# Kernel optimization log

Measured on AMD Instinct MI355X. Metric: run time of the kernel, lower is better.

Reference implementation:

```python
import jax, jax.numpy as jnp
import numpy as np

N_DATASETS = 2
DATASET_CATS = (1536, 1536)
TOTAL_CATS = 3072
MAX_UNIFY = 1536
N_NODES = TOTAL_CATS + MAX_UNIFY  # 4608
LRELU_ALPHA = 0.2
BI_TEMP = 0.05
NEG_INF = -9e15


def setup_inputs() -> dict:
    key = jax.random.key(0)
    ks = jax.random.split(key, 12)
    nfeat, nfeat_out, nfeat_adj, nhid, nheads = 512, 256, 64, 64, 4
    att_out, mlp = 256, 512
    s = lambda k, sh: (jax.random.normal(k, sh, jnp.float32) * 0.05)
    return {
        'x': jax.random.normal(ks[0], (N_NODES, nfeat), jnp.float32),
        'W_before': s(ks[1], (nfeat, nfeat_out)),
        'b_before': jnp.zeros((nfeat_out,), jnp.float32),
        'W_adj': s(ks[2], (nfeat_out, nfeat_adj)),
        'b_adj': jnp.zeros((nfeat_adj,), jnp.float32),
        'W_heads': s(ks[3], (nheads, nfeat_out, nhid)),
        'a_heads': s(ks[4], (nheads, 2 * nhid)),
        'W_out': s(ks[5], (nheads * nhid, att_out)),
        'a_out': s(ks[6], (2 * att_out,)),
        'W_lin1': s(ks[7], (att_out, mlp)),
        'b_lin1': jnp.zeros((mlp,), jnp.float32),
    }


def _calc_adjacency(x_out, W_adj, b_adj):
    # linear_adj + L2 normalize + cosine similarity + row normalization via diag(1/rowsum)
    af = x_out @ W_adj + b_adj                              # [N, nfeat_adj]
    nrm = jnp.sqrt(jnp.sum(af * af, axis=1, keepdims=True))
    naf = af / jnp.maximum(nrm, 1e-12)
    sim = naf @ naf.T                                       # [N, N]
    rowsum = jnp.sum(sim, axis=1)
    r_inv = 1.0 / rowsum
    r_inv = jnp.where(jnp.isinf(r_inv), 0.0, r_inv)
    return r_inv[:, None] * sim                             # diag(1/rowsum) @ sim


def _gat_multihead(x, adj, W, a):
    # W: [H, F, d], a: [H, 2d]. Standard pyGAT dense attention, vectorized over heads.
    d = W.shape[-1]
    Wh = jnp.einsum('nf,hfd->hnd', x, W)                    # [H, N, d]
    f1 = jnp.einsum('hnd,hd->hn', Wh, a[:, :d])             # [H, N]
    f2 = jnp.einsum('hnd,hd->hn', Wh, a[:, d:])             # [H, N]
    e = jax.nn.leaky_relu(f1[:, :, None] + f2[:, None, :], LRELU_ALPHA)  # [H, N, N]
    att = jnp.where(adj[None] > 0, e, NEG_INF)
    att = jax.nn.softmax(att, axis=-1)
    return jnp.einsum('hnm,hmd->hnd', att, Wh)              # [H, N, d]


def _gat_single(x, adj, W, a):
    d = W.shape[-1]
    Wh = x @ W                                              # [N, d]
    f1 = Wh @ a[:d]
    f2 = Wh @ a[d:]
    e = jax.nn.leaky_relu(f1[:, None] + f2[None, :], LRELU_ALPHA)
    att = jnp.where(adj > 0, e, NEG_INF)
    att = jax.nn.softmax(att, axis=-1)
    return att @ Wh


def reference(x, W_before, b_before, W_adj, b_adj, W_heads, a_heads, W_out, a_out, W_lin1, b_lin1):
    x1 = x @ W_before + b_before                            # linear_before
    adj = _calc_adjacency(x1, W_adj, b_adj)                 # before relu, as in source
    x1 = jax.nn.relu(x1)
    # multi-head GAT layer 1 (concat=True -> elu per head, concat along feature dim)
    h = jax.nn.elu(_gat_multihead(x1, adj, W_heads, a_heads))   # [H, N, d]
    H, N, d = h.shape
    feat = jnp.transpose(h, (1, 0, 2)).reshape(N, H * d)
    x2 = feat + x1                                          # residual; dropout is eval no-op
    # output attention head (concat=False -> no elu inside)
    x3 = jax.nn.elu(_gat_single(x2, adj, W_out, a_out) + x2)
    feat_mlp = x3 @ W_lin1 + b_lin1                          # linear1
    # sep_bipartite_graphs: per-dataset column-softmax over unify columns
    bgs = []
    cur = 0
    for nc in DATASET_CATS:
        blk = adj[cur:cur + nc, TOTAL_CATS:]                 # [nc, MAX_UNIFY]
        bgs.append(jax.nn.softmax(blk / BI_TEMP, axis=0))
        cur += nc
    return (feat_mlp[TOTAL_CATS:],) + tuple(bgs)


if __name__ == '__main__':
    out = reference(**setup_inputs())
    for o in out:
        print(o.shape, o.dtype)
```

## Files before the change

### kernel.cpp

```cpp
#include <hip/hip_runtime.h>
#include <hip/hip_bf16.h>
#include <math.h>

constexpr int NTOT = 4608;
constexpr int TC   = 3072;
constexpr int MU   = 1536;
constexpr int NH   = 4;

constexpr long OFF_ADJ  = 0;
constexpr long OFF_X1   = OFF_ADJ  + (long)NTOT*NTOT;
constexpr long OFF_NAF  = OFF_X1   + (long)NTOT*256;
constexpr long OFF_PART = OFF_NAF  + (long)NTOT*64;
constexpr long OFF_RINV = OFF_PART + 72*64;
constexpr long OFF_WH   = OFF_RINV + NTOT;
constexpr long OFF_F1H  = OFF_WH   + (long)4*NTOT*64;
constexpr long OFF_F2H  = OFF_F1H  + (long)4*NTOT;
constexpr long OFF_MXH  = OFF_F2H  + (long)4*NTOT;
constexpr long OFF_CIH  = OFF_MXH  + (long)4*NTOT;
constexpr long OFF_X2   = OFF_CIH  + (long)4*NTOT;
constexpr long OFF_WH2  = OFF_X2   + (long)NTOT*256;
constexpr long OFF_F1S  = OFF_WH2  + (long)NTOT*256;
constexpr long OFF_F2S  = OFF_F1S  + NTOT;
constexpr long OFF_MXS  = OFF_F2S  + NTOT;
constexpr long OFF_CIS  = OFF_MXS  + NTOT;
constexpr long OFF_X3   = OFF_CIS  + NTOT;
constexpr long OFF_PMAX = OFF_X3   + (long)MU*256;
constexpr long OFF_PSUM = OFF_PMAX + (long)2*12*MU;
constexpr long OFF_FMAX = OFF_PSUM + (long)2*12*MU;
constexpr long OFF_FIS  = OFF_FMAX + (long)2*MU;
constexpr long OFF_L1   = OFF_FIS  + (long)2*MU;
constexpr long OFF_L2   = OFF_L1   + (long)4*NTOT;
constexpr long OFF_PARTS = OFF_ADJ + (long)TC*NTOT;
constexpr long OFF_POSB  = OFF_PARTS + 2L*NTOT*36;
constexpr long OFF_MASKB = OFF_POSB  + 2L*NTOT*72;

typedef __attribute__((ext_vector_type(8))) short bf16x8;
typedef __attribute__((ext_vector_type(8))) unsigned short ushort8;
typedef __attribute__((ext_vector_type(4))) float floatx4;

__device__ __forceinline__ float elu(float x)   { return (x > 0.f) ? x : expm1f(x); }
__device__ __forceinline__ unsigned short f2bf(float f) {
    unsigned u = __float_as_uint(f);
    u += 0x7FFFu + ((u >> 16) & 1u);
    return (unsigned short)(u >> 16);
}

__global__ __launch_bounds__(256) void zero2_k(
    float* __restrict__ a, long na4, float* __restrict__ b, long nb4)
{
    long i = (long)blockIdx.x * 256 + threadIdx.x;
    float4 z = make_float4(0.f, 0.f, 0.f, 0.f);
    if (i < na4) *(float4*)(a + i * 4) = z;
    else {
        long j = i - na4;
        if (j < nb4) *(float4*)(b + j * 4) = z;
    }
}

template<bool RELU_A, bool BIAS>
__global__ __launch_bounds__(256) void gemm_rm(
    const float* __restrict__ A, const float* __restrict__ B,
    const float* __restrict__ bias, float* __restrict__ C,
    int K, int M, long strideBz, long strideCz)
{
    __shared__ float As[16][68];
    __shared__ float Bs[16][68];
    const float* Bz = B + (long)blockIdx.z * strideBz;
    float* Cz = C + (long)blockIdx.z * strideCz;
    int tid = threadIdx.x;
    int r0 = blockIdx.x * 64;
    int c0 = blockIdx.y * 64;
    int ty = tid >> 4, tx = tid & 15;
    int srow = tid >> 2, skg = tid & 3;
    int bkk = tid >> 4, bc4 = (tid & 15) * 4;
    const float* Arow = A + (long)(r0 + srow) * K + skg * 4;
    float4 aReg = *(const float4*)(Arow);
    float4 bReg = *(const float4*)&Bz[(long)bkk * M + c0 + bc4];
    float acc[4][4] = {};
    for (int k0 = 0; k0 < K; k0 += 16) {
        {
            float4 v = aReg;
            if (RELU_A) {
                v.x = fmaxf(v.x, 0.f); v.y = fmaxf(v.y, 0.f);
                v.z = fmaxf(v.z, 0.f); v.w = fmaxf(v.w, 0.f);
            }
            As[skg * 4 + 0][srow] = v.x;
            As[skg * 4 + 1][srow] = v.y;
            As[skg * 4 + 2][srow] = v.z;
            As[skg * 4 + 3][srow] = v.w;
            *(float4*)&Bs[bkk][bc4] = bReg;
        }
        __syncthreads();
        if (k0 + 16 < K) {
            aReg = *(const float4*)(Arow + k0 + 16);
            bReg = *(const float4*)&Bz[(long)(k0 + 16 + bkk) * M + c0 + bc4];
        }
        #pragma unroll
        for (int kk = 0; kk < 16; ++kk) {
            float4 av = *(const float4*)&As[kk][ty * 4];
            float4 bv = *(const float4*)&Bs[kk][tx * 4];
            float a[4] = { av.x, av.y, av.z, av.w };
            float b[4] = { bv.x, bv.y, bv.z, bv.w };
            #pragma unroll
            for (int i = 0; i < 4; ++i)
                #pragma unroll
                for (int j = 0; j < 4; ++j) acc[i][j] += a[i] * b[j];
        }
        __syncthreads();
    }
    #pragma unroll
    for (int i = 0; i < 4; ++i) {
        int r = r0 + ty * 4 + i;
        #pragma unroll
        for (int j = 0; j < 4; ++j) {
            int c = c0 + tx * 4 + j;
            float v = acc[i][j];
            if (BIAS) v += bias[c];
            Cz[(long)r * M + c] = v;
        }
    }
}

__global__ __launch_bounds__(256) void af_naf(
    const float* __restrict__ x1, const float* __restrict__ W_adj,
    const float* __restrict__ b_adj, float* __restrict__ nafT)
{
    __shared__ float rowbuf[4][256];
    int tid = threadIdx.x, w = tid >> 6, lane = tid & 63;
    int n = blockIdx.x * 4 + w;
    #pragma unroll
    for (int l = 0; l < 4; ++l) rowbuf[w][l * 64 + lane] = x1[(long)n * 256 + l * 64 + lane];
    __syncthreads();
    float acc = b_adj[lane];
    for (int k = 0; k < 256; ++k) acc += rowbuf[w][k] * W_adj[k * 64 + lane];
    float sq = acc * acc;
    #pragma unroll
    for (int off = 32; off >= 1; off >>= 1) sq += __shfl_xor(sq, off);
    float nrm = fmaxf(sqrtf(sq), 1e-12f);
    nafT[(long)lane * NTOT + n] = acc / nrm;
}

__global__ __launch_bounds__(256) void sim_k8(
    const float* __restrict__ nafT, float* __restrict__ sim,
    double* __restrict__ parts, unsigned long long* __restrict__ posb)
{
    __shared__ float As[32][128];
    __shared__ float Bs[32][128];
    __shared__ unsigned char sgn[128][2][16];
    int tid = threadIdx.x;
    int n0 = blockIdx.x * 128, m0 = blockIdx.y * 128;
    int ty = tid >> 4, tx = tid & 15;
    float acc[2][2][4][4] = {};
    for (int ks = 0; ks < 2; ++ks) {
        if (ks) __syncthreads();
        int k0 = ks * 32;
        #pragma unroll
        for (int l = 0; l < 4; ++l) {
            int idx = l * 256 + tid;
            int kk = idx >> 5, f4 = idx & 31;
            *(float4*)&As[kk][f4 * 4] = *(const float4*)&nafT[(long)(k0 + kk) * NTOT + n0 + f4 * 4];
            *(float4*)&Bs[kk][f4 * 4] = *(const float4*)&nafT[(long)(k0 + kk) * NTOT + m0 + f4 * 4];
        }
        __syncthreads();
        for (int kk = 0; kk < 32; ++kk) {
            float4 av0 = *(const float4*)&As[kk][ty * 4];
            float4 av1 = *(const float4*)&As[kk][64 + ty * 4];
            float4 bv0 = *(const float4*)&Bs[kk][tx * 4];
            float4 bv1 = *(const float4*)&Bs[kk][64 + tx * 4];
            float a[2][4] = { { av0.x, av0.y, av0.z, av0.w }, { av1.x, av1.y, av1.z, av1.w } };
            float b[2][4] = { { bv0.x, bv0.y, bv0.z, bv0.w }, { bv1.x, bv1.y, bv1.z, bv1.w } };
            #pragma unroll
            for (int rh = 0; rh < 2; ++rh)
                #pragma unroll
                for (int ch = 0; ch < 2; ++ch)
                    #pragma unroll
                    for (int i = 0; i < 4; ++i)
                        #pragma unroll
                        for (int j = 0; j < 4; ++j)
                            acc[rh][ch][i][j] += a[rh][i] * b[ch][j];
        }
    }
    if (m0 >= TC && n0 < TC) {
        #pragma unroll
        for (int rh = 0; rh < 2; ++rh)
            #pragma unroll
            for (int i = 0; i < 4; ++i) {
                long r = n0 + rh * 64 + ty * 4 + i;
                #pragma unroll
                for (int ch = 0; ch < 2; ++ch) {
                    float4 o = make_float4(acc[rh][ch][i][0], acc[rh][ch][i][1],
                                           acc[rh][ch][i][2], acc[rh][ch][i][3]);
                    *(float4*)(sim + r * NTOT + m0 + ch * 64 + tx * 4) = o;
                }
            }
    }
    int mt36 = m0 >> 7;
    #pragma unroll
    for (int rh = 0; rh < 2; ++rh)
        #pragma unroll
        for (int i = 0; i < 4; ++i) {
            double t = 0.0;
            #pragma unroll
            for (int ch = 0; ch < 2; ++ch)
                t += ((double)acc[rh][ch][i][0] + (double)acc[rh][ch][i][1])
                   + ((double)acc[rh][ch][i][2] + (double)acc[rh][ch][i][3]);
            #pragma unroll
            for (int off = 1; off < 16; off <<= 1) t += __shfl_xor(t, off);
            if (tx == 0)
                parts[(long)(n0 + rh * 64 + ty * 4 + i) * 36 + mt36] = t;
        }
    int mt = m0 >> 6;
    #pragma unroll
    for (int rh = 0; rh < 2; ++rh)
        #pragma unroll
        for (int i = 0; i < 4; ++i)
            #pragma unroll
            for (int ch = 0; ch < 2; ++ch) {
                unsigned nib = (unsigned)(acc[rh][ch][i][0] > 0.f)
                             | ((unsigned)(acc[rh][ch][i][1] > 0.f) << 1)
                             | ((unsigned)(acc[rh][ch][i][2] > 0.f) << 2)
                             | ((unsigned)(acc[rh][ch][i][3] > 0.f) << 3);
                sgn[rh * 64 + ty * 4 + i][ch][tx] = (unsigned char)nib;
            }
    __syncthreads();
    {
        int rl = tid >> 1, gh = tid & 1;
        unsigned long long w = 0;
        #pragma unroll
        for (int t = 0; t < 16; ++t)
            w |= (unsigned long long)sgn[rl][gh][t] << (4 * t);
        posb[(long)(n0 + rl) * 72 + mt + gh] = w;
    }
}

__global__ __launch_bounds__(256) void fused1(
    const float* __restrict__ Wh, unsigned short* __restrict__ Wf1,
    const float* __restrict__ a_heads,
    float* __restrict__ f1, float* __restrict__ f2,
    float* __restrict__ e2p, float* __restrict__ e2n,
    const double* __restrict__ parts, const unsigned long long* __restrict__ posb,
    float* __restrict__ rinv, unsigned long long* __restrict__ maskb)
{
    __shared__ float t[64][65];
    int b = blockIdx.x;
    int tid = threadIdx.x;
    if (b < 288) {
        int mt = b % 72, h = b / 72;
        int n0 = mt * 64;
        const float* inz = Wh + (long)h * NTOT * 64;
        int r4 = tid >> 6, k = tid & 63;
        #pragma unroll
        for (int l = 0; l < 16; ++l) {
            int row = l * 4 + r4;
            t[row][k] = inz[(long)(n0 + row) * 64 + k];
        }
        __syncthreads();
        #pragma unroll
        for (int q = 0; q < 2; ++q) {
            int fid = q * 256 + tid;
            int dt = fid >> 7, ks = (fid >> 6) & 1, lane = fid & 63;
            int mb = ks * 32 + (lane >> 4) * 8;
            int d  = dt * 16 + (lane & 15);
            ushort8 w;
            #pragma unroll
            for (int j = 0; j < 8; ++j) w[j] = f2bf(t[mb + j][d]);
            long idx = ((((long)(h * 72 + mt) * 4 + dt) * 2 + ks) * 64 + lane) * 8;
            *(ushort8*)&Wf1[idx] = w;
        }
    } else if (b < 288 + 4608) {
        int tb = b - 288;
        int xb = tb % 1152, h = tb / 1152;
        int w = tid >> 6, lane = tid & 63;
        int n = xb * 4 + w;
        const float* row = Wh + ((long)h * NTOT + n) * 64;
        const float* a1 = a_heads + (long)h * 128;
        const float* a2 = a1 + 64;
        float v = row[lane];
        float p1 = v * a1[lane];
        float p2 = v * a2[lane];
        #pragma unroll
        for (int off = 32; off >= 1; off >>= 1) { p1 += __shfl_xor(p1, off); p2 += __shfl_xor(p2, off); }
        if (lane == 0) {
            f1[(long)h * NTOT + n] = p1;
            f2[(long)h * NTOT + n] = p2;
            e2p[(long)h * NTOT + n] = __expf(p2);
            e2n[(long)h * NTOT + n] = __expf(0.2f * p2);
        }
    } else {
        int xb = b - (288 + 4608);
        int w = tid >> 6, lane = tid & 63;
        int n = xb * 4 + w;
        double s = (lane < 36) ? parts[(long)n * 36 + lane] : 0.0;
        #pragma unroll
        for (int off = 32; off >= 1; off >>= 1) s += __shfl_xor(s, off);
        float rs = (float)s;
        float r = 1.0f / rs;
        if (isinf(r)) r = 0.f;
        if (lane == 0) rinv[n] = r;
        unsigned long long pw = posb[(long)n * 72 + lane];
        unsigned long long mw = (r < 0.f) ? ~pw : pw;
        if (r == 0.f) mw = 0ull;
        maskb[(long)n * 72 + lane] = mw;
        if (lane < 8) {
            pw = posb[(long)n * 72 + 64 + lane];
            mw = (r < 0.f) ? ~pw : pw;
            if (r == 0.f) mw = 0ull;
            maskb[(long)n * 72 + 64 + lane] = mw;
        }
    }
}

__global__ __launch_bounds__(256) void fused2(
    const float* __restrict__ Wh2, unsigned short* __restrict__ Wf2,
    const float* __restrict__ a_out,
    float* __restrict__ f1, float* __restrict__ f2,
    float* __restrict__ e2p, float* __restrict__ e2n)
{
    __shared__ float t[64][65];
    int b = blockIdx.x;
    int tid = threadIdx.x;
    if (b < 288) {
        int mt = b % 72, by = b / 72;
        int n0 = mt * 64, d0 = by * 64;
        int r4 = tid >> 6, k = tid & 63;
        #pragma unroll
        for (int l = 0; l < 16; ++l) {
            int row = l * 4 + r4;
            t[row][k] = Wh2[(long)(n0 + row) * 256 + d0 + k];
        }
        __syncthreads();
        #pragma unroll
        for (int q = 0; q < 2; ++q) {
            int fid = q * 256 + tid;
            int ctl = fid >> 7, ks = (fid >> 6) & 1, lane = fid & 63;
            int mb = ks * 32 + (lane >> 4) * 8;
            int dl = ctl * 16 + (lane & 15);
            ushort8 w;
            #pragma unroll
            for (int j = 0; j < 8; ++j) w[j] = f2bf(t[mb + j][dl]);
            long idx = (((long)(mt * 16 + by * 4 + ctl) * 2 + ks) * 64 + lane) * 8;
            *(ushort8*)&Wf2[idx] = w;
        }
    } else {
        int xb = b - 288;
        int w = tid >> 6, lane = tid & 63;
        int n = xb * 4 + w;
        const float* row = Wh2 + (long)n * 256;
        const float* a1 = a_out;
        const float* a2 = a_out + 256;
        float p1 = 0.f, p2 = 0.f;
        #pragma unroll
        for (int l = 0; l < 4; ++l) {
            float v = row[l * 64 + lane];
            p1 += v * a1[l * 64 + lane];
            p2 += v * a2[l * 64 + lane];
        }
        #pragma unroll
        for (int off = 32; off >= 1; off >>= 1) { p1 += __shfl_xor(p1, off); p2 += __shfl_xor(p2, off); }
        if (lane == 0) {
            f1[n] = p1;
            f2[n] = p2;
            e2p[n] = __expf(p2);
            e2n[n] = __expf(0.2f * p2);
        }
    }
}

__global__ __launch_bounds__(256) void mh_attn(
    const unsigned long long* __restrict__ maskb,
    const float* __restrict__ f1,
    const float* __restrict__ e2p, const float* __restrict__ e2n,
    const unsigned short* __restrict__ Wf1, float* __restrict__ accb,
    float* __restrict__ lbuf)
{
    int tid = threadIdx.x;
    int wave = tid >> 6, lane = tid & 63;
    int n0 = blockIdx.x * 64;
    int h = blockIdx.y, ch = blockIdx.z;
    const float* Ep = e2p + (long)h * NTOT;
    const float* En = e2n + (long)h * NTOT;
    int arow = lane & 15, acol8 = (lane >> 4) * 8;
    int n = n0 + 16 * wave + arow;
    float r1 = f1[(long)h * NTOT + n];
    float e1p = __expf(r1), e1n = __expf(0.2f * r1);
    float lsum = 0.f;
    floatx4 acc[4] = {};
    for (int mt = ch * 12; mt < ch * 12 + 12; ++mt) {
        int m0 = mt * 64;
        bf16x8 bfr[2][4];
        #pragma unroll
        for (int ks = 0; ks < 2; ++ks)
            #pragma unroll
            for (int dt = 0; dt < 4; ++dt) {
                long idx = ((((long)(h * 72 + mt) * 4 + dt) * 2 + ks) * 64 + lane) * 8;
                bfr[ks][dt] = *(const bf16x8*)&Wf1[idx];
            }
        unsigned long long mw = maskb[(long)n * 72 + mt];
        bf16x8 afr[2];
        #pragma unroll
        for (int ks = 0; ks < 2; ++ks) {
            int mc = m0 + ks * 32 + acol8;
            float4 pv0 = *(const float4*)(Ep + mc);
            float4 pv1 = *(const float4*)(Ep + mc + 4);
            float4 nv0 = *(const float4*)(En + mc);
            float4 nv1 = *(const float4*)(En + mc + 4);
            unsigned bits = (unsigned)(mw >> (ks * 32 + acol8)) & 0xFFu;
            float fp[8] = { pv0.x, pv0.y, pv0.z, pv0.w, pv1.x, pv1.y, pv1.z, pv1.w };
            float fn[8] = { nv0.x, nv0.y, nv0.z, nv0.w, nv1.x, nv1.y, nv1.z, nv1.w };
            #pragma unroll
            for (int j = 0; j < 8; ++j) {
                float tp = e1p * fp[j];
                float tn = e1n * fn[j];
                float p = (tp >= 1.0f) ? tp : tn;
                p = ((bits >> j) & 1u) ? p : 0.f;
                lsum += p;
                afr[ks][j] = (short)f2bf(p);
            }
        }
        #pragma unroll
        for (int ks = 0; ks < 2; ++ks)
            #pragma unroll
            for (int dt = 0; dt < 4; ++dt)
                acc[dt] = __builtin_amdgcn_mfma_f32_16x16x32_bf16(afr[ks], bfr[ks][dt], acc[dt], 0, 0, 0);
    }
    lsum += __shfl_xor(lsum, 16);
    lsum += __shfl_xor(lsum, 32);
    if (lane < 16) atomicAdd(lbuf + (long)h * NTOT + n0 + 16 * wave + lane, lsum);
    int crow = n0 + 16 * wave + (lane >> 4) * 4;
    int ccol = h * 64 + (lane & 15);
    #pragma unroll
    for (int dt = 0; dt < 4; ++dt)
        #pragma unroll
        for (int r = 0; r < 4; ++r)
            atomicAdd(accb + (long)(crow + r) * 256 + ccol + dt * 16, acc[dt][r]);
}

__global__ __launch_bounds__(256) void mh_fin(
    const float* __restrict__ accb, const float* __restrict__ lbuf,
    float* __restrict__ x1, float* __restrict__ x2)
{
    long idx = ((long)blockIdx.x * 256 + threadIdx.x) * 4;
    long r = idx >> 8;
    int h = (int)((idx & 255) >> 6);
    float l = lbuf[(long)h * NTOT + r];
    float inv = (l > 0.f) ? 1.0f / l : 0.f;
    float4 a = *(const float4*)(accb + idx);
    float4 xv = *(const float4*)(x1 + idx);
    float4 o;
    o.x = elu(a.x * inv) + fmaxf(xv.x, 0.f);
    o.y = elu(a.y * inv) + fmaxf(xv.y, 0.f);
    o.z = elu(a.z * inv) + fmaxf(xv.z, 0.f);
    o.w = elu(a.w * inv) + fmaxf(xv.w, 0.f);
    *(float4*)(x2 + idx) = o;
    if (idx < (long)MU * 256)
        *(float4*)(x1 + idx) = make_float4(0.f, 0.f, 0.f, 0.f);
}

__global__ __launch_bounds__(256) void s_attn(
    const unsigned long long* __restrict__ maskb,
    const float* __restrict__ f1,
    const float* __restrict__ e2p, const float* __restrict__ e2n,
    const unsigned short* __restrict__ Wf2, float* __restrict__ accb,
    float* __restrict__ lbuf)
{
    int tid = threadIdx.x;
    int wave = tid >> 6, lane = tid & 63;
    int lr0 = blockIdx.x * 32;
    int by = blockIdx.y;
    int ch = blockIdx.z;
    int arow = lane & 15, acol8 = (lane >> 4) * 8;
    int rt = wave & 1;
    int dt0 = (wave >> 1) * 4;
    int n = TC + lr0 + 16 * rt + arow;
    float r1 = f1[n];
    float e1p = __expf(r1), e1n = __expf(0.2f * r1);
    float lsum = 0.f;
    floatx4 acc[4] = {};
    for (int mt = ch * 6; mt < ch * 6 + 6; ++mt) {
        int m0 = mt * 64;
        bf16x8 bfr[2][4];
        #pragma unroll
        for (int ks = 0; ks < 2; ++ks)
            #pragma unroll
            for (int t = 0; t < 4; ++t) {
                long idx = (((long)(mt * 16 + by * 8 + dt0 + t) * 2 + ks) * 64 + lane) * 8;
                bfr[ks][t] = *(const bf16x8*)&Wf2[idx];
            }
        unsigned long long mw = maskb[(long)n * 72 + mt];
        bf16x8 afr[2];
        #pragma unroll
        for (int ks = 0; ks < 2; ++ks) {
            int mc = m0 + ks * 32 + acol8;
            float4 pv0 = *(const float4*)(e2p + mc);
            float4 pv1 = *(const float4*)(e2p + mc + 4);
            float4 nv0 = *(const float4*)(e2n + mc);
            float4 nv1 = *(const float4*)(e2n + mc + 4);
            unsigned bits = (unsigned)(mw >> (ks * 32 + acol8)) & 0xFFu;
            float fp[8] = { pv0.x, pv0.y, pv0.z, pv0.w, pv1.x, pv1.y, pv1.z, pv1.w };
            float fn[8] = { nv0.x, nv0.y, nv0.z, nv0.w, nv1.x, nv1.y, nv1.z, nv1.w };
            #pragma unroll
            for (int j = 0; j < 8; ++j) {
                float tp = e1p * fp[j];
                float tn = e1n * fn[j];
                float p = (tp >= 1.0f) ? tp : tn;
                p = ((bits >> j) & 1u) ? p : 0.f;
                lsum += p;
                afr[ks][j] = (short)f2bf(p);
            }
        }
        #pragma unroll
        for (int ks = 0; ks < 2; ++ks)
            #pragma unroll
            for (int t = 0; t < 4; ++t)
                acc[t] = __builtin_amdgcn_mfma_f32_16x16x32_bf16(afr[ks], bfr[ks][t], acc[t], 0, 0, 0);
    }
    lsum += __shfl_xor(lsum, 16);
    lsum += __shfl_xor(lsum, 32);
    if (by == 0 && wave < 2 && lane < 16)
        atomicAdd(lbuf + lr0 + 16 * wave + lane, lsum);
    int crow = lr0 + 16 * rt + (lane >> 4) * 4;
    #pragma unroll
    for (int t = 0; t < 4; ++t) {
        int ccol = by * 128 + (dt0 + t) * 16 + (lane & 15);
        #pragma unroll
        for (int r = 0; r < 4; ++r)
            atomicAdd(accb + (long)(crow + r) * 256 + ccol, acc[t][r]);
    }
}

__global__ __launch_bounds__(256) void s_fin(
    const float* __restrict__ accb, const float* __restrict__ lbuf,
    const float* __restrict__ x2, float* __restrict__ x3)
{
    long idx = ((long)blockIdx.x * 256 + threadIdx.x) * 4;
    long r = idx >> 8;
    float l = lbuf[r];
    float inv = (l > 0.f) ? 1.0f / l : 0.f;
    float4 a = *(const float4*)(accb + idx);
    float4 xv = *(const float4*)(x2 + (long)TC * 256 + idx);
    float4 o;
    o.x = elu(a.x * inv + xv.x);
    o.y = elu(a.y * inv + xv.y);
    o.z = elu(a.z * inv + xv.z);
    o.w = elu(a.w * inv + xv.w);
    *(float4*)(x3 + idx) = o;
}

__global__ __launch_bounds__(256) void bi_partial(
    const float* __restrict__ sim, const float* __restrict__ rinv,
    float* __restrict__ pmax, float* __restrict__ psum)
{
    int c = blockIdx.x * 256 + threadIdx.x;
    int ch = blockIdx.y;
    int ds = blockIdx.z;
    float m = -3.0e38f, s = 0.f;
    int rbase = ds * MU + ch * 128;
    for (int r = 0; r < 128; ++r) {
        float a = sim[(long)(rbase + r) * NTOT + TC + c] * rinv[rbase + r];
        float v = a * 20.0f;
        if (v <= m) s += expf(v - m);
        else { s = s * expf(m - v) + 1.f; m = v; }
    }
    pmax[((long)ds * 12 + ch) * MU + c] = m;
    psum[((long)ds * 12 + ch) * MU + c] = s;
}

__global__ __launch_bounds__(256) void bi_combine(
    const float* __restrict__ pmax, const float* __restrict__ psum,
    float* __restrict__ fmax, float* __restrict__ fis)
{
    int b = blockIdx.x;
    int ds = b / 6, ct = b % 6;
    int c = ct * 256 + threadIdx.x;
    float m = -3.0e38f;
    for (int ch = 0; ch < 12; ++ch) m = fmaxf(m, pmax[((long)ds * 12 + ch) * MU + c]);
    float s = 0.f;
    for (int ch = 0; ch < 12; ++ch)
        s += psum[((long)ds * 12 + ch) * MU + c] * expf(pmax[((long)ds * 12 + ch) * MU + c] - m);
    fmax[ds * MU + c] = m;
    fis[ds * MU + c] = 1.0f / s;
}

__global__ __launch_bounds__(256) void bi_norm(
    const float* __restrict__ sim, const float* __restrict__ rinv,
    const float* __restrict__ fmax, const float* __restrict__ fis,
    float* __restrict__ outbg)
{
    int c = blockIdx.x * 256 + threadIdx.x;
    int ch = blockIdx.y;
    int ds = blockIdx.z;
    float m = fmax[ds * MU + c], inv = fis[ds * MU + c];
    long obase = (long)ds * MU * MU;
    int rbase = ch * 128;
    for (int r = 0; r < 128; ++r) {
        int row = ds * MU + rbase + r;
        float a = sim[(long)row * NTOT + TC + c] * rinv[row];
        float v = a * 20.0f;
        outbg[obase + (long)(rbase + r) * MU + c] = expf(v - m) * inv;
    }
}

extern "C" void kernel_launch(void* const* d_in, const int* in_sizes, int n_in,
                              void* d_out, int out_size, void* d_ws, size_t ws_size,
                              hipStream_t stream)
{
    const float* x        = (const float*)d_in[0];
    const float* W_before = (const float*)d_in[1];
    const float* b_before = (const float*)d_in[2];
    const float* W_adj    = (const float*)d_in[3];
    const float* b_adj    = (const float*)d_in[4];
    const float* W_heads  = (const float*)d_in[5];
    const float* a_heads  = (const float*)d_in[6];
    const float* W_out    = (const float*)d_in[7];
    const float* a_out    = (const float*)d_in[8];
    const float* W_lin1   = (const float*)d_in[9];
    const float* b_lin1   = (const float*)d_in[10];
    float* out = (float*)d_out;
    float* ws  = (float*)d_ws;

    float* sim  = ws + OFF_ADJ;
    float* x1p  = ws + OFF_X1;
    float* nafT = ws + OFF_NAF;
    float* rinv = ws + OFF_RINV;
    float* Wh   = ws + OFF_WH;
    float* f1h  = ws + OFF_F1H;
    float* f2h  = ws + OFF_F2H;
    float* e2ph = ws + OFF_MXH;
    float* e2nh = ws + OFF_CIH;
    float* x2   = ws + OFF_X2;
    float* Wh2  = ws + OFF_WH2;
    float* f1s  = ws + OFF_F1S;
    float* f2s  = ws + OFF_F2S;
    float* e2sp = ws + OFF_MXS;
    float* e2sn = ws + OFF_CIS;
    float* x3   = ws + OFF_X3;
    float* pmax = ws + OFF_PMAX;
    float* psum = ws + OFF_PSUM;
    float* fmx  = ws + OFF_FMAX;
    float* fis  = ws + OFF_FIS;
    float* l1   = ws + OFF_L1;
    float* l2   = ws + OFF_L2;
    float* acc1 = ws + OFF_WH2;
    float* acc2 = ws + OFF_X1;
    unsigned short* Wf1 = (unsigned short*)(ws + OFF_X2);
    unsigned short* Wf2 = (unsigned short*)(ws + OFF_X1 + (long)MU * 256);
    double* parts = (double*)(ws + OFF_PARTS);
    unsigned long long* posb  = (unsigned long long*)(ws + OFF_POSB);
    unsigned long long* maskb = (unsigned long long*)(ws + OFF_MASKB);

    dim3 b256(256);

    zero2_k<<<dim3(1172), b256, 0, stream>>>(acc1, (long)NTOT * 64, l1, 5120);
    gemm_rm<false, true><<<dim3(72, 4, 1), b256, 0, stream>>>(x, W_before, b_before, x1p, 512, 256, 0, 0);
    af_naf<<<dim3(1152), b256, 0, stream>>>(x1p, W_adj, b_adj, nafT);
    sim_k8<<<dim3(36, 36), b256, 0, stream>>>(nafT, sim, parts, posb);
    gemm_rm<true, false><<<dim3(72, 1, 4), b256, 0, stream>>>(x1p, W_heads, nullptr, Wh, 256, 64,
                                                              (long)256 * 64, (long)NTOT * 64);
    fused1<<<dim3(288 + 4608 + 1152), b256, 0, stream>>>(Wh, Wf1, a_heads, f1h, f2h, e2ph, e2nh,
                                                         parts, posb, rinv, maskb);
    mh_attn<<<dim3(72, 4, 6), b256, 0, stream>>>(maskb, f1h, e2ph, e2nh, Wf1, acc1, l1);
    mh_fin<<<dim3(NTOT * 256 / 1024), b256, 0, stream>>>(acc1, l1, x1p, x2);
    gemm_rm<false, false><<<dim3(72, 4, 1), b256, 0, stream>>>(x2, W_out, nullptr, Wh2, 256, 256, 0, 0);
    fused2<<<dim3(288 + 1152), b256, 0, stream>>>(Wh2, Wf2, a_out, f1s, f2s, e2sp, e2sn);
    s_attn<<<dim3(48, 2, 12), b256, 0, stream>>>(maskb, f1s, e2sp, e2sn, Wf2, acc2, l2);
    s_fin<<<dim3(MU * 256 / 1024), b256, 0, stream>>>(acc2, l2, x2, x3);
    gemm_rm<false, true><<<dim3(24, 8, 1), b256, 0, stream>>>(x3, W_lin1, b_lin1, out, 256, 512, 0, 0);
    bi_partial<<<dim3(6, 12, 2), b256, 0, stream>>>(sim, rinv, pmax, psum);
    bi_combine<<<dim3(12), b256, 0, stream>>>(pmax, psum, fmx, fis);
    bi_norm<<<dim3(6, 12, 2), b256, 0, stream>>>(sim, rinv, fmx, fis, out + (long)MU * 512);
}
```

Before: 380.3 us.

## Transpose attention mask layout and software-prefetch next tile in attention kernels

The attention mask is now stored tile-major (mask tile index by node) so that lanes reading consecutive nodes fetch contiguous 64-bit words, instead of the row-major layout with a 72-word stride. Both attention kernels fully unroll their tile loops and load the next tile's bf16 B fragments and mask word into registers while the current tile's softmax weights and MFMAs are computed. This double-buffering hides global load latency at the cost of extra VGPRs, which could reduce occupancy.

```diff
diff --git a/kernel.cpp b/kernel.cpp
--- a/kernel.cpp
+++ b/kernel.cpp
@@ -239,7 +239,7 @@
     float* __restrict__ f1, float* __restrict__ f2,
     float* __restrict__ e2p, float* __restrict__ e2n,
     const double* __restrict__ parts, const unsigned long long* __restrict__ posb,
-    float* __restrict__ rinv, unsigned long long* __restrict__ maskb)
+    float* __restrict__ rinv, unsigned long long* __restrict__ maskT)
 {
     __shared__ float t[64][65];
     int b = blockIdx.x;
@@ -300,12 +300,12 @@
         unsigned long long pw = posb[(long)n * 72 + lane];
         unsigned long long mw = (r < 0.f) ? ~pw : pw;
         if (r == 0.f) mw = 0ull;
-        maskb[(long)n * 72 + lane] = mw;
+        maskT[(long)lane * NTOT + n] = mw;
         if (lane < 8) {
             pw = posb[(long)n * 72 + 64 + lane];
             mw = (r < 0.f) ? ~pw : pw;
             if (r == 0.f) mw = 0ull;
-            maskb[(long)n * 72 + 64 + lane] = mw;
+            maskT[(long)(64 + lane) * NTOT + n] = mw;
         }
     }
 }
@@ -367,7 +367,7 @@
 }
 
 __global__ __launch_bounds__(256) void mh_attn(
-    const unsigned long long* __restrict__ maskb,
+    const unsigned long long* __restrict__ maskT,
     const float* __restrict__ f1,
     const float* __restrict__ e2p, const float* __restrict__ e2n,
     const unsigned short* __restrict__ Wf1, float* __restrict__ accb,
@@ -385,17 +385,18 @@
     float e1p = __expf(r1), e1n = __expf(0.2f * r1);
     float lsum = 0.f;
     floatx4 acc[4] = {};
-    for (int mt = ch * 12; mt < ch * 12 + 12; ++mt) {
+    int mt0 = ch * 12;
+    bf16x8 bfr[2][4];
+    #pragma unroll
+    for (int ks = 0; ks < 2; ++ks)
+        #pragma unroll
+        for (int dt = 0; dt < 4; ++dt)
+            bfr[ks][dt] = *(const bf16x8*)&Wf1[((((long)(h * 72 + mt0) * 4 + dt) * 2 + ks) * 64 + lane) * 8];
+    unsigned long long mw = maskT[(long)mt0 * NTOT + n];
+    #pragma unroll
+    for (int i = 0; i < 12; ++i) {
+        int mt = mt0 + i;
         int m0 = mt * 64;
-        bf16x8 bfr[2][4];
-        #pragma unroll
-        for (int ks = 0; ks < 2; ++ks)
-            #pragma unroll
-            for (int dt = 0; dt < 4; ++dt) {
-                long idx = ((((long)(h * 72 + mt) * 4 + dt) * 2 + ks) * 64 + lane) * 8;
-                bfr[ks][dt] = *(const bf16x8*)&Wf1[idx];
-            }
-        unsigned long long mw = maskb[(long)n * 72 + mt];
         bf16x8 afr[2];
         #pragma unroll
         for (int ks = 0; ks < 2; ++ks) {
@@ -417,11 +418,33 @@
                 afr[ks][j] = (short)f2bf(p);
             }
         }
+        bf16x8 nb[2][4];
+        unsigned long long nm = mw;
+        if (i < 11) {
+            nm = maskT[(long)(mt + 1) * NTOT + n];
+            #pragma unroll
+            for (int ks = 0; ks < 2; ++ks)
+                #pragma unroll
+                for (int dt = 0; dt < 4; ++dt)
+                    nb[ks][dt] = *(const bf16x8*)&Wf1[((((long)(h * 72 + mt + 1) * 4 + dt) * 2 + ks) * 64 + lane) * 8];
+        } else {
+            #pragma unroll
+            for (int ks = 0; ks < 2; ++ks)
+                #pragma unroll
+                for (int dt = 0; dt < 4; ++dt)
+                    nb[ks][dt] = bfr[ks][dt];
+        }
         #pragma unroll
         for (int ks = 0; ks < 2; ++ks)
             #pragma unroll
             for (int dt = 0; dt < 4; ++dt)
                 acc[dt] = __builtin_amdgcn_mfma_f32_16x16x32_bf16(afr[ks], bfr[ks][dt], acc[dt], 0, 0, 0);
+        #pragma unroll
+        for (int ks = 0; ks < 2; ++ks)
+            #pragma unroll
+            for (int dt = 0; dt < 4; ++dt)
+                bfr[ks][dt] = nb[ks][dt];
+        mw = nm;
     }
     lsum += __shfl_xor(lsum, 16);
     lsum += __shfl_xor(lsum, 32);
@@ -457,7 +480,7 @@
 }
 
 __global__ __launch_bounds__(256) void s_attn(
-    const unsigned long long* __restrict__ maskb,
+    const unsigned long long* __restrict__ maskT,
     const float* __restrict__ f1,
     const float* __restrict__ e2p, const float* __restrict__ e2n,
     const unsigned short* __restrict__ Wf2, float* __restrict__ accb,
@@ -476,17 +499,18 @@
     float e1p = __expf(r1), e1n = __expf(0.2f * r1);
     float lsum = 0.f;
     floatx4 acc[4] = {};
-    for (int mt = ch * 6; mt < ch * 6 + 6; ++mt) {
+    int mt0 = ch * 6;
+    bf16x8 bfr[2][4];
+    #pragma unroll
+    for (int ks = 0; ks < 2; ++ks)
+        #pragma unroll
+        for (int t = 0; t < 4; ++t)
+            bfr[ks][t] = *(const bf16x8*)&Wf2[(((long)(mt0 * 16 + by * 8 + dt0 + t) * 2 + ks) * 64 + lane) * 8];
+    unsigned long long mw = maskT[(long)mt0 * NTOT + n];
+    #pragma unroll
+    for (int i = 0; i < 6; ++i) {
+        int mt = mt0 + i;
         int m0 = mt * 64;
-        bf16x8 bfr[2][4];
-        #pragma unroll
-        for (int ks = 0; ks < 2; ++ks)
-            #pragma unroll
-            for (int t = 0; t < 4; ++t) {
-                long idx = (((long)(mt * 16 + by * 8 + dt0 + t) * 2 + ks) * 64 + lane) * 8;
-                bfr[ks][t] = *(const bf16x8*)&Wf2[idx];
-            }
-        unsigned long long mw = maskb[(long)n * 72 + mt];
         bf16x8 afr[2];
         #pragma unroll
         for (int ks = 0; ks < 2; ++ks) {
@@ -508,11 +532,33 @@
                 afr[ks][j] = (short)f2bf(p);
             }
         }
+        bf16x8 nb[2][4];
+        unsigned long long nm = mw;
+        if (i < 5) {
+            nm = maskT[(long)(mt + 1) * NTOT + n];
+            #pragma unroll
+            for (int ks = 0; ks < 2; ++ks)
+                #pragma unroll
+                for (int t = 0; t < 4; ++t)
+                    nb[ks][t] = *(const bf16x8*)&Wf2[(((long)((mt + 1) * 16 + by * 8 + dt0 + t) * 2 + ks) * 64 + lane) * 8];
+        } else {
+            #pragma unroll
+            for (int ks = 0; ks < 2; ++ks)
+                #pragma unroll
+                for (int t = 0; t < 4; ++t)
+                    nb[ks][t] = bfr[ks][t];
+        }
         #pragma unroll
         for (int ks = 0; ks < 2; ++ks)
             #pragma unroll
             for (int t = 0; t < 4; ++t)
                 acc[t] = __builtin_amdgcn_mfma_f32_16x16x32_bf16(afr[ks], bfr[ks][t], acc[t], 0, 0, 0);
+        #pragma unroll
+        for (int ks = 0; ks < 2; ++ks)
+            #pragma unroll
+            for (int t = 0; t < 4; ++t)
+                bfr[ks][t] = nb[ks][t];
+        mw = nm;
     }
     lsum += __shfl_xor(lsum, 16);
     lsum += __shfl_xor(lsum, 32);
@@ -646,7 +692,7 @@
     unsigned short* Wf2 = (unsigned short*)(ws + OFF_X1 + (long)MU * 256);
     double* parts = (double*)(ws + OFF_PARTS);
     unsigned long long* posb  = (unsigned long long*)(ws + OFF_POSB);
-    unsigned long long* maskb = (unsigned long long*)(ws + OFF_MASKB);
+    unsigned long long* maskT = (unsigned long long*)(ws + OFF_MASKB);
 
     dim3 b256(256);
 
@@ -657,12 +703,12 @@
     gemm_rm<true, false><<<dim3(72, 1, 4), b256, 0, stream>>>(x1p, W_heads, nullptr, Wh, 256, 64,
                                                               (long)256 * 64, (long)NTOT * 64);
     fused1<<<dim3(288 + 4608 + 1152), b256, 0, stream>>>(Wh, Wf1, a_heads, f1h, f2h, e2ph, e2nh,
-                                                         parts, posb, rinv, maskb);
-    mh_attn<<<dim3(72, 4, 6), b256, 0, stream>>>(maskb, f1h, e2ph, e2nh, Wf1, acc1, l1);
+                                                         parts, posb, rinv, maskT);
+    mh_attn<<<dim3(72, 4, 6), b256, 0, stream>>>(maskT, f1h, e2ph, e2nh, Wf1, acc1, l1);
     mh_fin<<<dim3(NTOT * 256 / 1024), b256, 0, stream>>>(acc1, l1, x1p, x2);
     gemm_rm<false, false><<<dim3(72, 4, 1), b256, 0, stream>>>(x2, W_out, nullptr, Wh2, 256, 256, 0, 0);
     fused2<<<dim3(288 + 1152), b256, 0, stream>>>(Wh2, Wf2, a_out, f1s, f2s, e2sp, e2sn);
-    s_attn<<<dim3(48, 2, 12), b256, 0, stream>>>(maskb, f1s, e2sp, e2sn, Wf2, acc2, l2);
+    s_attn<<<dim3(48, 2, 12), b256, 0, stream>>>(maskT, f1s, e2sp, e2sn, Wf2, acc2, l2);
     s_fin<<<dim3(MU * 256 / 1024), b256, 0, stream>>>(acc2, l2, x2, x3);
     gemm_rm<false, true><<<dim3(24, 8, 1), b256, 0, stream>>>(x3, W_lin1, b_lin1, out, 256, 512, 0, 0);
     bi_partial<<<dim3(6, 12, 2), b256, 0, stream>>>(sim, rinv, pmax, psum);
```

Result: no change. 387.2 us (+1.8%).

## Transpose attention mask and give each wave two row groups to reuse B fragments

Applied to the files above, without the earlier changes.

The bitmask is now stored column-tile-major (maskT[mt][n]), so the per-tile mask loads in the attention kernels are contiguous across rows. Each wave now processes 32 query rows (two 16-row groups) and reuses the loaded Wf B-fragments and exp vectors for both groups. This halves the grid and the redundant B-fragment and exp loads. The cost is more accumulator registers per wave and fewer blocks. s_attn's column split is also reorganised to 4 groups of 64 columns.

```diff
diff --git a/kernel.cpp b/kernel.cpp
--- a/kernel.cpp
+++ b/kernel.cpp
@@ -239,7 +239,7 @@
     float* __restrict__ f1, float* __restrict__ f2,
     float* __restrict__ e2p, float* __restrict__ e2n,
     const double* __restrict__ parts, const unsigned long long* __restrict__ posb,
-    float* __restrict__ rinv, unsigned long long* __restrict__ maskb)
+    float* __restrict__ rinv, unsigned long long* __restrict__ maskT)
 {
     __shared__ float t[64][65];
     int b = blockIdx.x;
@@ -300,12 +300,12 @@
         unsigned long long pw = posb[(long)n * 72 + lane];
         unsigned long long mw = (r < 0.f) ? ~pw : pw;
         if (r == 0.f) mw = 0ull;
-        maskb[(long)n * 72 + lane] = mw;
+        maskT[(long)lane * NTOT + n] = mw;
         if (lane < 8) {
             pw = posb[(long)n * 72 + 64 + lane];
             mw = (r < 0.f) ? ~pw : pw;
             if (r == 0.f) mw = 0ull;
-            maskb[(long)n * 72 + 64 + lane] = mw;
+            maskT[(long)(64 + lane) * NTOT + n] = mw;
         }
     }
 }
@@ -367,7 +367,7 @@
 }
 
 __global__ __launch_bounds__(256) void mh_attn(
-    const unsigned long long* __restrict__ maskb,
+    const unsigned long long* __restrict__ maskT,
     const float* __restrict__ f1,
     const float* __restrict__ e2p, const float* __restrict__ e2n,
     const unsigned short* __restrict__ Wf1, float* __restrict__ accb,
@@ -375,28 +375,33 @@
 {
     int tid = threadIdx.x;
     int wave = tid >> 6, lane = tid & 63;
-    int n0 = blockIdx.x * 64;
+    int n0 = blockIdx.x * 128 + wave * 32;
     int h = blockIdx.y, ch = blockIdx.z;
     const float* Ep = e2p + (long)h * NTOT;
     const float* En = e2n + (long)h * NTOT;
     int arow = lane & 15, acol8 = (lane >> 4) * 8;
-    int n = n0 + 16 * wave + arow;
-    float r1 = f1[(long)h * NTOT + n];
-    float e1p = __expf(r1), e1n = __expf(0.2f * r1);
-    float lsum = 0.f;
-    floatx4 acc[4] = {};
-    for (int mt = ch * 12; mt < ch * 12 + 12; ++mt) {
+    float e1p[2], e1n[2], lsum[2] = {};
+    #pragma unroll
+    for (int g = 0; g < 2; ++g) {
+        float r1 = f1[(long)h * NTOT + n0 + 16 * g + arow];
+        e1p[g] = __expf(r1);
+        e1n[g] = __expf(0.2f * r1);
+    }
+    floatx4 acc[2][4] = {};
+    int mt0 = ch * 12;
+    for (int i = 0; i < 12; ++i) {
+        int mt = mt0 + i;
         int m0 = mt * 64;
+        unsigned long long mw[2];
+        #pragma unroll
+        for (int g = 0; g < 2; ++g)
+            mw[g] = maskT[(long)mt * NTOT + n0 + 16 * g + arow];
         bf16x8 bfr[2][4];
         #pragma unroll
         for (int ks = 0; ks < 2; ++ks)
             #pragma unroll
-            for (int dt = 0; dt < 4; ++dt) {
-                long idx = ((((long)(h * 72 + mt) * 4 + dt) * 2 + ks) * 64 + lane) * 8;
-                bfr[ks][dt] = *(const bf16x8*)&Wf1[idx];
-            }
-        unsigned long long mw = maskb[(long)n * 72 + mt];
-        bf16x8 afr[2];
+            for (int dt = 0; dt < 4; ++dt)
+                bfr[ks][dt] = *(const bf16x8*)&Wf1[((((long)(h * 72 + mt) * 4 + dt) * 2 + ks) * 64 + lane) * 8];
         #pragma unroll
         for (int ks = 0; ks < 2; ++ks) {
             int mc = m0 + ks * 32 + acol8;
@@ -404,35 +409,41 @@
             float4 pv1 = *(const float4*)(Ep + mc + 4);
             float4 nv0 = *(const float4*)(En + mc);
             float4 nv1 = *(const float4*)(En + mc + 4);
-            unsigned bits = (unsigned)(mw >> (ks * 32 + acol8)) & 0xFFu;
             float fp[8] = { pv0.x, pv0.y, pv0.z, pv0.w, pv1.x, pv1.y, pv1.z, pv1.w };
             float fn[8] = { nv0.x, nv0.y, nv0.z, nv0.w, nv1.x, nv1.y, nv1.z, nv1.w };
             #pragma unroll
-            for (int j = 0; j < 8; ++j) {
-                float tp = e1p * fp[j];
-                float tn = e1n * fn[j];
-                float p = (tp >= 1.0f) ? tp : tn;
-                p = ((bits >> j) & 1u) ? p : 0.f;
-                lsum += p;
-                afr[ks][j] = (short)f2bf(p);
+            for (int g = 0; g < 2; ++g) {
+                unsigned bits = (unsigned)(mw[g] >> (ks * 32 + acol8)) & 0xFFu;
+                bf16x8 afr;
+                #pragma unroll
+                for (int j = 0; j < 8; ++j) {
+                    float tp = e1p[g] * fp[j];
+                    float tn = e1n[g] * fn[j];
+                    float p = (tp >= 1.0f) ? tp : tn;
+                    p = ((bits >> j) & 1u) ? p : 0.f;
+                    lsum[g] += p;
+                    afr[j] = (short)f2bf(p);
+                }
+                #pragma unroll
+                for (int dt = 0; dt < 4; ++dt)
+                    acc[g][dt] = __builtin_amdgcn_mfma_f32_16x16x32_bf16(afr, bfr[ks][dt], acc[g][dt], 0, 0, 0);
             }
         }
-        #pragma unroll
-        for (int ks = 0; ks < 2; ++ks)
-            #pragma unroll
-            for (int dt = 0; dt < 4; ++dt)
-                acc[dt] = __builtin_amdgcn_mfma_f32_16x16x32_bf16(afr[ks], bfr[ks][dt], acc[dt], 0, 0, 0);
-    }
-    lsum += __shfl_xor(lsum, 16);
-    lsum += __shfl_xor(lsum, 32);
-    if (lane < 16) atomicAdd(lbuf + (long)h * NTOT + n0 + 16 * wave + lane, lsum);
-    int crow = n0 + 16 * wave + (lane >> 4) * 4;
-    int ccol = h * 64 + (lane & 15);
-    #pragma unroll
-    for (int dt = 0; dt < 4; ++dt)
-        #pragma unroll
-        for (int r = 0; r < 4; ++r)
-            atomicAdd(accb + (long)(crow + r) * 256 + ccol + dt * 16, acc[dt][r]);
+    }
+    #pragma unroll
+    for (int g = 0; g < 2; ++g) {
+        float ls = lsum[g];
+        ls += __shfl_xor(ls, 16);
+        ls += __shfl_xor(ls, 32);
+        if (lane < 16) atomicAdd(lbuf + (long)h * NTOT + n0 + 16 * g + lane, ls);
+        int crow = n0 + 16 * g + (lane >> 4) * 4;
+        int ccol = h * 64 + (lane & 15);
+        #pragma unroll
+        for (int dt = 0; dt < 4; ++dt)
+            #pragma unroll
+            for (int r = 0; r < 4; ++r)
+                atomicAdd(accb + (long)(crow + r) * 256 + ccol + dt * 16, acc[g][dt][r]);
+    }
 }
 
 __global__ __launch_bounds__(256) void mh_fin(
@@ -457,7 +468,7 @@
 }
 
 __global__ __launch_bounds__(256) void s_attn(
-    const unsigned long long* __restrict__ maskb,
+    const unsigned long long* __restrict__ maskT,
     const float* __restrict__ f1,
     const float* __restrict__ e2p, const float* __restrict__ e2n,
     const unsigned short* __restrict__ Wf2, float* __restrict__ accb,
@@ -465,29 +476,32 @@
 {
     int tid = threadIdx.x;
     int wave = tid >> 6, lane = tid & 63;
-    int lr0 = blockIdx.x * 32;
-    int by = blockIdx.y;
+    int lr0 = blockIdx.x * 128 + wave * 32;
+    int cg = blockIdx.y;
     int ch = blockIdx.z;
     int arow = lane & 15, acol8 = (lane >> 4) * 8;
-    int rt = wave & 1;
-    int dt0 = (wave >> 1) * 4;
-    int n = TC + lr0 + 16 * rt + arow;
-    float r1 = f1[n];
-    float e1p = __expf(r1), e1n = __expf(0.2f * r1);
-    float lsum = 0.f;
-    floatx4 acc[4] = {};
-    for (int mt = ch * 6; mt < ch * 6 + 6; ++mt) {
+    float e1p[2], e1n[2], lsum[2] = {};
+    #pragma unroll
+    for (int g = 0; g < 2; ++g) {
+        float r1 = f1[TC + lr0 + 16 * g + arow];
+        e1p[g] = __expf(r1);
+        e1n[g] = __expf(0.2f * r1);
+    }
+    floatx4 acc[2][4] = {};
+    int mt0 = ch * 6;
+    for (int i = 0; i < 6; ++i) {
+        int mt = mt0 + i;
         int m0 = mt * 64;
+        unsigned long long mw[2];
+        #pragma unroll
+        for (int g = 0; g < 2; ++g)
+            mw[g] = maskT[(long)mt * NTOT + TC + lr0 + 16 * g + arow];
         bf16x8 bfr[2][4];
         #pragma unroll
         for (int ks = 0; ks < 2; ++ks)
             #pragma unroll
-            for (int t = 0; t < 4; ++t) {
-                long idx = (((long)(mt * 16 + by * 8 + dt0 + t) * 2 + ks) * 64 + lane) * 8;
-                bfr[ks][t] = *(const bf16x8*)&Wf2[idx];
-            }
-        unsigned long long mw = maskb[(long)n * 72 + mt];
-        bf16x8 afr[2];
+            for (int t = 0; t < 4; ++t)
+                bfr[ks][t] = *(const bf16x8*)&Wf2[(((long)(mt * 16 + cg * 4 + t) * 2 + ks) * 64 + lane) * 8];
         #pragma unroll
         for (int ks = 0; ks < 2; ++ks) {
             int mc = m0 + ks * 32 + acol8;
@@ -495,36 +509,41 @@
             float4 pv1 = *(const float4*)(e2p + mc + 4);
             float4 nv0 = *(const float4*)(e2n + mc);
             float4 nv1 = *(const float4*)(e2n + mc + 4);
-            unsigned bits = (unsigned)(mw >> (ks * 32 + acol8)) & 0xFFu;
             float fp[8] = { pv0.x, pv0.y, pv0.z, pv0.w, pv1.x, pv1.y, pv1.z, pv1.w };
             float fn[8] = { nv0.x, nv0.y, nv0.z, nv0.w, nv1.x, nv1.y, nv1.z, nv1.w };
             #pragma unroll
-            for (int j = 0; j < 8; ++j) {
-                float tp = e1p * fp[j];
-                float tn = e1n * fn[j];
-                float p = (tp >= 1.0f) ? tp : tn;
-                p = ((bits >> j) & 1u) ? p : 0.f;
-                lsum += p;
-                afr[ks][j] = (short)f2bf(p);
+            for (int g = 0; g < 2; ++g) {
+                unsigned bits = (unsigned)(mw[g] >> (ks * 32 + acol8)) & 0xFFu;
+                bf16x8 afr;
+                #pragma unroll
+                for (int j = 0; j < 8; ++j) {
+                    float tp = e1p[g] * fp[j];
+                    float tn = e1n[g] * fn[j];
+                    float p = (tp >= 1.0f) ? tp : tn;
+                    p = ((bits >> j) & 1u) ? p : 0.f;
+                    lsum[g] += p;
+                    afr[j] = (short)f2bf(p);
+                }
+                #pragma unroll
+                for (int t = 0; t < 4; ++t)
+                    acc[g][t] = __builtin_amdgcn_mfma_f32_16x16x32_bf16(afr, bfr[ks][t], acc[g][t], 0, 0, 0);
             }
         }
-        #pragma unroll
-        for (int ks = 0; ks < 2; ++ks)
-            #pragma unroll
-            for (int t = 0; t < 4; ++t)
-                acc[t] = __builtin_amdgcn_mfma_f32_16x16x32_bf16(afr[ks], bfr[ks][t], acc[t], 0, 0, 0);
-    }
-    lsum += __shfl_xor(lsum, 16);
-    lsum += __shfl_xor(lsum, 32);
-    if (by == 0 && wave < 2 && lane < 16)
-        atomicAdd(lbuf + lr0 + 16 * wave + lane, lsum);
-    int crow = lr0 + 16 * rt + (lane >> 4) * 4;
-    #pragma unroll
-    for (int t = 0; t < 4; ++t) {
-        int ccol = by * 128 + (dt0 + t) * 16 + (lane & 15);
-        #pragma unroll
-        for (int r = 0; r < 4; ++r)
-            atomicAdd(accb + (long)(crow + r) * 256 + ccol, acc[t][r]);
+    }
+    #pragma unroll
+    for (int g = 0; g < 2; ++g) {
+        float ls = lsum[g];
+        ls += __shfl_xor(ls, 16);
+        ls += __shfl_xor(ls, 32);
+        if (cg == 0 && lane < 16) atomicAdd(lbuf + lr0 + 16 * g + lane, ls);
+        int crow = lr0 + 16 * g + (lane >> 4) * 4;
+        #pragma unroll
+        for (int t = 0; t < 4; ++t) {
+            int ccol = cg * 64 + t * 16 + (lane & 15);
+            #pragma unroll
+            for (int r = 0; r < 4; ++r)
+                atomicAdd(accb + (long)(crow + r) * 256 + ccol, acc[g][t][r]);
+        }
     }
 }
 
@@ -646,7 +665,7 @@
     unsigned short* Wf2 = (unsigned short*)(ws + OFF_X1 + (long)MU * 256);
     double* parts = (double*)(ws + OFF_PARTS);
     unsigned long long* posb  = (unsigned long long*)(ws + OFF_POSB);
-    unsigned long long* maskb = (unsigned long long*)(ws + OFF_MASKB);
+    unsigned long long* maskT = (unsigned long long*)(ws + OFF_MASKB);
 
     dim3 b256(256);
 
@@ -657,12 +676,12 @@
     gemm_rm<true, false><<<dim3(72, 1, 4), b256, 0, stream>>>(x1p, W_heads, nullptr, Wh, 256, 64,
                                                               (long)256 * 64, (long)NTOT * 64);
     fused1<<<dim3(288 + 4608 + 1152), b256, 0, stream>>>(Wh, Wf1, a_heads, f1h, f2h, e2ph, e2nh,
-                                                         parts, posb, rinv, maskb);
-    mh_attn<<<dim3(72, 4, 6), b256, 0, stream>>>(maskb, f1h, e2ph, e2nh, Wf1, acc1, l1);
+                                                         parts, posb, rinv, maskT);
+    mh_attn<<<dim3(36, 4, 6), b256, 0, stream>>>(maskT, f1h, e2ph, e2nh, Wf1, acc1, l1);
     mh_fin<<<dim3(NTOT * 256 / 1024), b256, 0, stream>>>(acc1, l1, x1p, x2);
     gemm_rm<false, false><<<dim3(72, 4, 1), b256, 0, stream>>>(x2, W_out, nullptr, Wh2, 256, 256, 0, 0);
     fused2<<<dim3(288 + 1152), b256, 0, stream>>>(Wh2, Wf2, a_out, f1s, f2s, e2sp, e2sn);
-    s_attn<<<dim3(48, 2, 12), b256, 0, stream>>>(maskb, f1s, e2sp, e2sn, Wf2, acc2, l2);
+    s_attn<<<dim3(12, 4, 12), b256, 0, stream>>>(maskT, f1s, e2sp, e2sn, Wf2, acc2, l2);
     s_fin<<<dim3(MU * 256 / 1024), b256, 0, stream>>>(acc2, l2, x2, x3);
     gemm_rm<false, true><<<dim3(24, 8, 1), b256, 0, stream>>>(x3, W_lin1, b_lin1, out, 256, 512, 0, 0);
     bi_partial<<<dim3(6, 12, 2), b256, 0, stream>>>(sim, rinv, pmax, psum);
```

After: 397.8 us. 1.05x slower.
